# Optimization experiments

Measured on AMD Instinct MI355X. Metric: run time of the kernel, lower is better.

The kernel has to match this reference:

```python
import jax, jax.numpy as jnp
import numpy as np

T = 8  # num_temp_tokens (init arg)
K = 3  # routing conv kernel size (hardcoded in module)


def setup_inputs() -> dict:
    key = jax.random.key(0)
    ks = jax.random.split(key, 7)
    C, CO, NE = 384, 1152, 4
    BT, N = 256, 197
    s = 0.02
    return {
        "x": jax.random.normal(ks[0], (BT, N, C), dtype=jnp.float32),
        "rf_w": jax.random.normal(ks[1], (NE, C), dtype=jnp.float32) * s,
        "rf_b": jax.random.normal(ks[2], (NE,), dtype=jnp.float32) * s,
        "moe_w": jax.random.normal(ks[3], (NE, CO, C, K), dtype=jnp.float32) * s,
        "moe_b": jax.random.normal(ks[4], (NE, CO), dtype=jnp.float32) * s,
        "weight": jax.random.normal(ks[5], (CO, C), dtype=jnp.float32) * s,
        "bias": jax.random.normal(ks[6], (CO,), dtype=jnp.float32) * s,
    }


def _routing(cls, rf_w, rf_b, moe_w, moe_b):
    # cls: (b, C, T). route_func_linear_cls_token_moe forward.
    pooled = cls.mean(axis=2)                       # global avg pool over T -> (b, C)
    rf = pooled @ rf_w.T + rf_b                     # 1x1 conv -> (b, num_experts)
    w = jnp.einsum('be,eock->bock', rf, moe_w)      # per-sample mixed weights (b, 3C, C, K)
    br = rf @ moe_b                                 # per-sample mixed bias (b, 3C)
    clsp = jnp.pad(cls, ((0, 0), (0, 0), (K // 2, K // 2)))
    # sliding windows over T: (b, C, T, K)
    clsw = jnp.stack([clsp[:, :, k:k + cls.shape[2]] for k in range(K)], axis=-1)
    routing = jnp.einsum('bock,bctk->bot', w, clsw) + br[:, :, None] + 1.0  # (b, 3C, T)
    return routing


def reference(x, rf_w, rf_b, moe_w, moe_b, weight, bias):
    bt, n, C = x.shape
    b = bt // T
    xb = x.reshape(b, T, n, C)                      # '(b t) n c -> b t n c'
    cls = xb[:, :, 0, :].transpose(0, 2, 1)         # (b, C, T) cls token stream
    routing = _routing(cls, rf_w, rf_b, moe_w, moe_b)  # (b, 3C, T)
    r = routing.transpose(0, 2, 1)                  # (b, T, 3C)
    rq, rk, rv = jnp.split(r, 3, axis=-1)           # each (b, T, C)
    Wq, Wk, Wv = jnp.split(weight, 3, axis=0)       # each (C, C)
    bq, bk, bv = jnp.split(bias, 3)                 # each (C,)

    def branch(rr, Wc, bc):
        # grouped 1x1 conv with per-(b,t) cin-scaled weight:
        # out[b,t,o,n] = sum_c Wc[o,c] * rr[b,t,c] * x[b,t,n,c] + bc[o]*rr[b,t,o]
        xs = xb * rr[:, :, None, :]                 # (b, T, n, C)
        return jnp.einsum('btnc,oc->bton', xs, Wc) + (bc[None, None, :] * rr)[..., None]

    oq = branch(rq, Wq, bq)
    ok = branch(rk, Wk, bk)
    ov = branch(rv, Wv, bv)
    out = jnp.concatenate([oq, ok, ov], axis=2)     # (b, T, 3C, n)
    return out.reshape(bt, 3 * C, n)
```

## Files before the change

### kernel.cpp

```cpp
#include <hip/hip_runtime.h>
#include <hip/hip_bf16.h>

typedef __attribute__((ext_vector_type(8))) short short8;
typedef __attribute__((ext_vector_type(4))) short short4v;
typedef __attribute__((ext_vector_type(4))) float f32x4;

__device__ __forceinline__ short f2bf(float f) {
    union { float f; unsigned u; } v; v.f = f;
    unsigned r = v.u + 0x7FFF + ((v.u >> 16) & 1);
    return (short)(r >> 16);
}

__device__ __forceinline__ void gll16(const short* g, short* l) {
    __builtin_amdgcn_global_load_lds(
        (const __attribute__((address_space(1))) void*)g,
        (__attribute__((address_space(3))) void*)l, 16, 0, 0);
}

#define NE 4
#define CC 384
#define CO 1152
#define TT 8
#define NN 197
#define NB 32
#define BT 256
#define MOEW_ELEMS 5308416
#define W_ELEMS    442368

__global__ __launch_bounds__(256) void prep_kernel(
    const float* __restrict__ x, const float* __restrict__ rf_w,
    const float* __restrict__ rf_b, const float* __restrict__ moe_w,
    const float* __restrict__ weight,
    short* __restrict__ moeWb, short* __restrict__ Wb,
    short* __restrict__ Yb, float* __restrict__ rf)
{
    int blk = blockIdx.x, tid = threadIdx.x;
    if (blk < NB) {
        __shared__ float clsL[TT * CC];
        __shared__ float pooled[CC];
        int b = blk;
        for (int flat = tid; flat < TT * CC; flat += 256) {
            int t = flat / CC, c = flat - t * CC;
            clsL[flat] = x[(size_t)(b * TT + t) * NN * CC + c];
        }
        __syncthreads();
        for (int c = tid; c < CC; c += 256) {
            float s = 0.f;
            #pragma unroll
            for (int t = 0; t < TT; t++) s += clsL[t * CC + c];
            pooled[c] = s * 0.125f;
        }
        for (int t = 0; t < TT; t++)
            for (int flat = tid; flat < CC * 3; flat += 256) {
                int c = flat / 3, k = flat - c * 3;
                int u = t + k - 1;
                float v = (u >= 0 && u < TT) ? clsL[u * CC + c] : 0.f;
                Yb[(size_t)(b * TT + t) * (CC * 3) + flat] = f2bf(v);
            }
        __syncthreads();
        int wave = tid >> 6, lane = tid & 63;
        float p = 0.f;
        for (int c = lane; c < CC; c += 64) p += pooled[c] * rf_w[wave * CC + c];
        #pragma unroll
        for (int off = 32; off; off >>= 1) p += __shfl_down(p, off, 64);
        if (lane == 0) rf[b * NE + wave] = p + rf_b[wave];
    } else {
        const long NU = (MOEW_ELEMS + W_ELEMS) / 4;
        long step = (long)(gridDim.x - NB) * 256;
        for (long unit = (long)(blk - NB) * 256 + tid; unit < NU; unit += step) {
            long idx = unit * 4;
            float4 v; short* dst;
            if (idx < MOEW_ELEMS) { v = *(const float4*)(moe_w + idx); dst = moeWb + idx; }
            else { long j = idx - MOEW_ELEMS; v = *(const float4*)(weight + j); dst = Wb + j; }
            short4v s;
            s.x = f2bf(v.x); s.y = f2bf(v.y); s.z = f2bf(v.z); s.w = f2bf(v.w);
            *(short4v*)dst = s;
        }
    }
}

__global__ __launch_bounds__(256) void gemm_P(
    const short* __restrict__ A, const short* __restrict__ B, float* __restrict__ P)
{
    __shared__ short A_lds[64 * 64];
    __shared__ short B_lds[64 * 64];
    int bm = blockIdx.x, bn = blockIdx.y, tid = threadIdx.x;
    int wave = tid >> 6, lane = tid & 63, l15 = lane & 15, lq = lane >> 4;
    f32x4 acc[4];
    #pragma unroll
    for (int j = 0; j < 4; j++) acc[j] = (f32x4){0.f, 0.f, 0.f, 0.f};

    for (int kk = 0; kk < 1152 / 64; kk++) {
        __syncthreads();
        #pragma unroll
        for (int j2 = 0; j2 < 2; j2++) {
            int flat = j2 * 256 + tid;
            int row = flat >> 3, seg = flat & 7;
            gll16(A + (size_t)(bm * 64 + row) * 1152 + kk * 64 + seg * 8, &A_lds[flat * 8]);
            gll16(B + (size_t)(bn * 64 + row) * 1152 + kk * 64 + seg * 8, &B_lds[flat * 8]);
        }
        __syncthreads();
        #pragma unroll
        for (int ks = 0; ks < 2; ks++) {
            short8 a = *(short8*)&A_lds[(wave * 16 + l15) * 64 + ks * 32 + lq * 8];
            #pragma unroll
            for (int j = 0; j < 4; j++) {
                short8 bfr = *(short8*)&B_lds[(j * 16 + l15) * 64 + ks * 32 + lq * 8];
                acc[j] = __builtin_amdgcn_mfma_f32_16x16x32_bf16(a, bfr, acc[j], 0, 0, 0);
            }
        }
    }
    #pragma unroll
    for (int j = 0; j < 4; j++)
        #pragma unroll
        for (int reg = 0; reg < 4; reg++) {
            int row = bm * 64 + wave * 16 + lq * 4 + reg;
            int col = bn * 64 + j * 16 + l15;
            P[(size_t)row * 256 + col] = acc[j][reg];
        }
}

__global__ __launch_bounds__(256) void combine_kernel(
    const float* __restrict__ P, const float* __restrict__ rf,
    const float* __restrict__ moe_b, float* __restrict__ r_ws)
{
    __shared__ float rf_l[NB * NE];
    int o = blockIdx.x, tid = threadIdx.x;
    if (tid < NB * NE) rf_l[tid] = rf[tid];
    __syncthreads();
    int b = tid >> 3;
    float acc = 1.0f;
    #pragma unroll
    for (int e = 0; e < NE; e++)
        acc += rf_l[b * NE + e] * (P[(size_t)(e * CO + o) * 256 + tid] + moe_b[e * CO + o]);
    r_ws[(size_t)tid * CO + o] = acc;
}

__global__ __launch_bounds__(256) void main_gemm_fused(
    const float* __restrict__ x, const short* __restrict__ Wb,
    const float* __restrict__ r_ws, const float* __restrict__ bias,
    float* __restrict__ out)
{
    __shared__ short A_lds[2][128 * 32];
    __shared__ short B_lds[2][112 * 32];

    int g = blockIdx.x;
    int u = g & 7, w2 = g >> 3;
    int mt = w2 % 9;
    int pq = u + 8 * (w2 / 9);
    int bt = pq >> 1, nt = pq & 1;
    int tid = threadIdx.x;
    int br = mt / 3;

    const short* Abase = Wb + (size_t)(mt * 128) * CC;

    int wave = tid >> 6, lane = tid & 63, l15 = lane & 15, lq = lane >> 4;
    int oct = tid & 3;
    int rbase = tid >> 2;

    const float* xbase = x + ((size_t)bt * NN + nt * 112) * CC + oct * 8;
    const float* rbp   = r_ws + (size_t)bt * CO + br * CC + oct * 8;

    f32x4 acc[2][7];
    #pragma unroll
    for (int i = 0; i < 2; i++)
        #pragma unroll
        for (int j = 0; j < 7; j++) acc[i][j] = (f32x4){0.f, 0.f, 0.f, 0.f};

    float4 xr[4];
    float4 rr0, rr1;

    auto prefetch = [&](int t) {
        rr0 = *(const float4*)(rbp + t * 32);
        rr1 = *(const float4*)(rbp + t * 32 + 4);
        #pragma unroll
        for (int j2 = 0; j2 < 2; j2++) {
            int row = j2 * 64 + rbase;
            float4 z = {0.f, 0.f, 0.f, 0.f};
            xr[2 * j2] = z; xr[2 * j2 + 1] = z;
            if ((j2 == 0 || rbase < 48) && nt * 112 + row < NN) {
                const float* p = xbase + (size_t)row * CC + t * 32;
                xr[2 * j2]     = *(const float4*)p;
                xr[2 * j2 + 1] = *(const float4*)(p + 4);
            }
        }
    };
    auto issueA = [&](int t, int buf) {
        #pragma unroll
        for (int j2 = 0; j2 < 2; j2++) {
            int flat = j2 * 256 + tid;
            int row = flat >> 2, ss = flat & 3;
            int seg = ss ^ ((row >> 1) & 3);
            gll16(Abase + (size_t)row * CC + t * 32 + seg * 8, &A_lds[buf][flat * 8]);
        }
    };

    prefetch(0);
    issueA(0, 0);

    for (int t = 0; t < 12; t++) {
        int pb = t & 1;
        {
            short* Bd = &B_lds[pb][0];
            #pragma unroll
            for (int j2 = 0; j2 < 2; j2++) {
                int row = j2 * 64 + rbase;
                if (j2 == 0 || rbase < 48) {
                    int ss = oct ^ ((row >> 1) & 3);
                    float4 a = xr[2 * j2], b = xr[2 * j2 + 1];
                    short8 s;
                    s[0] = f2bf(a.x * rr0.x); s[1] = f2bf(a.y * rr0.y);
                    s[2] = f2bf(a.z * rr0.z); s[3] = f2bf(a.w * rr0.w);
                    s[4] = f2bf(b.x * rr1.x); s[5] = f2bf(b.y * rr1.y);
                    s[6] = f2bf(b.z * rr1.z); s[7] = f2bf(b.w * rr1.w);
                    *(short8*)&Bd[row * 32 + ss * 8] = s;
                }
            }
        }
        __syncthreads();
        if (t < 11) {
            prefetch(t + 1);
            issueA(t + 1, pb ^ 1);
        }
        {
            int sx = lq ^ ((l15 >> 1) & 3);
            short8 a0 = *(short8*)&A_lds[pb][(wave * 32      + l15) * 32 + sx * 8];
            short8 a1 = *(short8*)&A_lds[pb][(wave * 32 + 16 + l15) * 32 + sx * 8];
            #pragma unroll
            for (int j = 0; j < 7; j++) {
                short8 bfr = *(short8*)&B_lds[pb][(j * 16 + l15) * 32 + sx * 8];
                acc[0][j] = __builtin_amdgcn_mfma_f32_16x16x32_bf16(a0, bfr, acc[0][j], 0, 0, 0);
                acc[1][j] = __builtin_amdgcn_mfma_f32_16x16x32_bf16(a1, bfr, acc[1][j], 0, 0, 0);
            }
        }
    }

    size_t outbase = (size_t)bt * (CO * NN);
    #pragma unroll
    for (int mi = 0; mi < 2; mi++)
        #pragma unroll
        for (int reg = 0; reg < 4; reg++) {
            int o = mt * 128 + wave * 32 + mi * 16 + lq * 4 + reg;
            float bo = bias[o] * r_ws[(size_t)bt * CO + o];
            #pragma unroll
            for (int j = 0; j < 7; j++) {
                int n = nt * 112 + j * 16 + l15;
                if (n < NN) out[outbase + (size_t)o * NN + n] = acc[mi][j][reg] + bo;
            }
        }
}

extern "C" void kernel_launch(void* const* d_in, const int* in_sizes, int n_in,
                              void* d_out, int out_size, void* d_ws, size_t ws_size,
                              hipStream_t stream) {
    const float* x      = (const float*)d_in[0];
    const float* rf_w   = (const float*)d_in[1];
    const float* rf_b   = (const float*)d_in[2];
    const float* moe_w  = (const float*)d_in[3];
    const float* moe_b  = (const float*)d_in[4];
    const float* weight = (const float*)d_in[5];
    const float* bias   = (const float*)d_in[6];
    float* out = (float*)d_out;

    char* ws = (char*)d_ws;
    short* Wb    = (short*)(ws + 0);
    short* moeWb = (short*)(ws + 884736);
    short* Yb    = (short*)(ws + 11501568);
    float* rf    = (float*)(ws + 12091392);
    float* P     = (float*)(ws + 12091904);
    float* r_ws  = (float*)(ws + 16810496);

    prep_kernel<<<512, 256, 0, stream>>>(x, rf_w, rf_b, moe_w, weight, moeWb, Wb, Yb, rf);
    gemm_P<<<dim3(72, 4), 256, 0, stream>>>(moeWb, Yb, P);
    combine_kernel<<<1152, 256, 0, stream>>>(P, rf, moe_b, r_ws);
    main_gemm_fused<<<4608, 256, 0, stream>>>(x, Wb, r_ws, bias, out);
}
```

Baseline: 451.1 us.

## Split main GEMM tile across 8 waves with 512-thread blocks

The main fused GEMM kernel now launches 512 threads per block instead of 256. Each of the 8 waves computes one 16-row slice of the 128-row output tile instead of two, and the staging and A-load work is spread so each thread handles a single row segment. This halves per-thread accumulators and load work to raise per-block parallelism and latency hiding. The cost is fewer blocks resident per CU, heavier block-wide barriers, and an idle tail of 64 threads during B staging. Each wave also reuses every B fragment for only one MFMA instead of two, so LDS reads per MFMA go up.

Measured after the change: 485.9 us. 7.7% more time.

```diff
diff --git a/kernel.cpp b/kernel.cpp
--- a/kernel.cpp
+++ b/kernel.cpp
@@ -136,7 +136,7 @@
     r_ws[(size_t)tid * CO + o] = acc;
 }
 
-__global__ __launch_bounds__(256) void main_gemm_fused(
+__global__ __launch_bounds__(512) void main_gemm_fused(
     const float* __restrict__ x, const short* __restrict__ Wb,
     const float* __restrict__ r_ws, const float* __restrict__ bias,
     float* __restrict__ out)
@@ -157,41 +157,54 @@
     int wave = tid >> 6, lane = tid & 63, l15 = lane & 15, lq = lane >> 4;
     int oct = tid & 3;
     int rbase = tid >> 2;
+    bool stager = (tid < 448);
 
     const float* xbase = x + ((size_t)bt * NN + nt * 112) * CC + oct * 8;
     const float* rbp   = r_ws + (size_t)bt * CO + br * CC + oct * 8;
 
-    f32x4 acc[2][7];
-    #pragma unroll
-    for (int i = 0; i < 2; i++)
-        #pragma unroll
-        for (int j = 0; j < 7; j++) acc[i][j] = (f32x4){0.f, 0.f, 0.f, 0.f};
-
-    float4 xr[4];
+    f32x4 acc[7];
+    #pragma unroll
+    for (int j = 0; j < 7; j++) acc[j] = (f32x4){0.f, 0.f, 0.f, 0.f};
+
+    float4 xr0, xr1;
     float4 rr0, rr1;
 
     auto prefetch = [&](int t) {
-        rr0 = *(const float4*)(rbp + t * 32);
-        rr1 = *(const float4*)(rbp + t * 32 + 4);
-        #pragma unroll
-        for (int j2 = 0; j2 < 2; j2++) {
-            int row = j2 * 64 + rbase;
+        if (stager) {
+            rr0 = *(const float4*)(rbp + t * 32);
+            rr1 = *(const float4*)(rbp + t * 32 + 4);
             float4 z = {0.f, 0.f, 0.f, 0.f};
-            xr[2 * j2] = z; xr[2 * j2 + 1] = z;
-            if ((j2 == 0 || rbase < 48) && nt * 112 + row < NN) {
-                const float* p = xbase + (size_t)row * CC + t * 32;
-                xr[2 * j2]     = *(const float4*)p;
-                xr[2 * j2 + 1] = *(const float4*)(p + 4);
+            xr0 = z; xr1 = z;
+            if (nt * 112 + rbase < NN) {
+                const float* p = xbase + (size_t)rbase * CC + t * 32;
+                xr0 = *(const float4*)p;
+                xr1 = *(const float4*)(p + 4);
             }
         }
     };
     auto issueA = [&](int t, int buf) {
-        #pragma unroll
-        for (int j2 = 0; j2 < 2; j2++) {
-            int flat = j2 * 256 + tid;
-            int row = flat >> 2, ss = flat & 3;
-            int seg = ss ^ ((row >> 1) & 3);
-            gll16(Abase + (size_t)row * CC + t * 32 + seg * 8, &A_lds[buf][flat * 8]);
+        int row = tid >> 2, ss = tid & 3;
+        int seg = ss ^ ((row >> 1) & 3);
+        gll16(Abase + (size_t)row * CC + t * 32 + seg * 8, &A_lds[buf][tid * 8]);
+    };
+    auto stageB = [&](int pb) {
+        if (stager) {
+            int ss = oct ^ ((rbase >> 1) & 3);
+            short8 s;
+            s[0] = f2bf(xr0.x * rr0.x); s[1] = f2bf(xr0.y * rr0.y);
+            s[2] = f2bf(xr0.z * rr0.z); s[3] = f2bf(xr0.w * rr0.w);
+            s[4] = f2bf(xr1.x * rr1.x); s[5] = f2bf(xr1.y * rr1.y);
+            s[6] = f2bf(xr1.z * rr1.z); s[7] = f2bf(xr1.w * rr1.w);
+            *(short8*)&B_lds[pb][rbase * 32 + ss * 8] = s;
+        }
+    };
+    auto compute = [&](int pb) {
+        int sx = lq ^ ((l15 >> 1) & 3);
+        short8 a = *(short8*)&A_lds[pb][(wave * 16 + l15) * 32 + sx * 8];
+        #pragma unroll
+        for (int j = 0; j < 7; j++) {
+            short8 bfr = *(short8*)&B_lds[pb][(j * 16 + l15) * 32 + sx * 8];
+            acc[j] = __builtin_amdgcn_mfma_f32_16x16x32_bf16(a, bfr, acc[j], 0, 0, 0);
         }
     };
 
@@ -200,54 +213,26 @@
 
     for (int t = 0; t < 12; t++) {
         int pb = t & 1;
-        {
-            short* Bd = &B_lds[pb][0];
-            #pragma unroll
-            for (int j2 = 0; j2 < 2; j2++) {
-                int row = j2 * 64 + rbase;
-                if (j2 == 0 || rbase < 48) {
-                    int ss = oct ^ ((row >> 1) & 3);
-                    float4 a = xr[2 * j2], b = xr[2 * j2 + 1];
-                    short8 s;
-                    s[0] = f2bf(a.x * rr0.x); s[1] = f2bf(a.y * rr0.y);
-                    s[2] = f2bf(a.z * rr0.z); s[3] = f2bf(a.w * rr0.w);
-                    s[4] = f2bf(b.x * rr1.x); s[5] = f2bf(b.y * rr1.y);
-                    s[6] = f2bf(b.z * rr1.z); s[7] = f2bf(b.w * rr1.w);
-                    *(short8*)&Bd[row * 32 + ss * 8] = s;
-                }
-            }
-        }
+        stageB(pb);
         __syncthreads();
         if (t < 11) {
             prefetch(t + 1);
             issueA(t + 1, pb ^ 1);
         }
-        {
-            int sx = lq ^ ((l15 >> 1) & 3);
-            short8 a0 = *(short8*)&A_lds[pb][(wave * 32      + l15) * 32 + sx * 8];
-            short8 a1 = *(short8*)&A_lds[pb][(wave * 32 + 16 + l15) * 32 + sx * 8];
-            #pragma unroll
-            for (int j = 0; j < 7; j++) {
-                short8 bfr = *(short8*)&B_lds[pb][(j * 16 + l15) * 32 + sx * 8];
-                acc[0][j] = __builtin_amdgcn_mfma_f32_16x16x32_bf16(a0, bfr, acc[0][j], 0, 0, 0);
-                acc[1][j] = __builtin_amdgcn_mfma_f32_16x16x32_bf16(a1, bfr, acc[1][j], 0, 0, 0);
-            }
-        }
+        compute(pb);
     }
 
     size_t outbase = (size_t)bt * (CO * NN);
     #pragma unroll
-    for (int mi = 0; mi < 2; mi++)
-        #pragma unroll
-        for (int reg = 0; reg < 4; reg++) {
-            int o = mt * 128 + wave * 32 + mi * 16 + lq * 4 + reg;
-            float bo = bias[o] * r_ws[(size_t)bt * CO + o];
-            #pragma unroll
-            for (int j = 0; j < 7; j++) {
-                int n = nt * 112 + j * 16 + l15;
-                if (n < NN) out[outbase + (size_t)o * NN + n] = acc[mi][j][reg] + bo;
-            }
-        }
+    for (int reg = 0; reg < 4; reg++) {
+        int o = mt * 128 + wave * 16 + lq * 4 + reg;
+        float bo = bias[o] * r_ws[(size_t)bt * CO + o];
+        #pragma unroll
+        for (int j = 0; j < 7; j++) {
+            int n = nt * 112 + j * 16 + l15;
+            if (n < NN) out[outbase + (size_t)o * NN + n] = acc[j][reg] + bo;
+        }
+    }
 }
 
 extern "C" void kernel_launch(void* const* d_in, const int* in_sizes, int n_in,
@@ -273,5 +258,5 @@
     prep_kernel<<<512, 256, 0, stream>>>(x, rf_w, rf_b, moe_w, weight, moeWb, Wb, Yb, rf);
     gemm_P<<<dim3(72, 4), 256, 0, stream>>>(moeWb, Yb, P);
     combine_kernel<<<1152, 256, 0, stream>>>(P, rf, moe_b, r_ws);
-    main_gemm_fused<<<4608, 256, 0, stream>>>(x, Wb, r_ws, bias, out);
-}
+    main_gemm_fused<<<4608, 512, 0, stream>>>(x, Wb, r_ws, bias, out);
+}
```

## Split-K the routing GEMM three ways and use packed bf16 conversion

Applied to the files above, without the earlier changes.

The routing GEMM over the mixed expert weights is split along K into three slices via a third grid dimension, so it launches 864 blocks instead of 288 and fills more compute units. Each slice writes partials to a larger workspace region, and the combine kernel sums them. Separately, the hand-written float-to-bf16 rounding is replaced with the packed v_cvt_pk_bf16_f32 instruction in the weight conversion and in the main GEMM's B staging. This costs extra partial-sum traffic and a bigger workspace.

After: 449.3 us. Within noise of the previous version (-0.4%).

```diff
diff --git a/kernel.cpp b/kernel.cpp
--- a/kernel.cpp
+++ b/kernel.cpp
@@ -9,6 +9,12 @@
     union { float f; unsigned u; } v; v.f = f;
     unsigned r = v.u + 0x7FFF + ((v.u >> 16) & 1);
     return (short)(r >> 16);
+}
+
+__device__ __forceinline__ unsigned cvtpk(float lo, float hi) {
+    unsigned r;
+    asm("v_cvt_pk_bf16_f32 %0, %1, %2" : "=v"(r) : "v"(lo), "v"(hi));
+    return r;
 }
 
 __device__ __forceinline__ void gll16(const short* g, short* l) {
@@ -24,6 +30,7 @@
 #define NN 197
 #define NB 32
 #define BT 256
+#define KS 3
 #define MOEW_ELEMS 5308416
 #define W_ELEMS    442368
 
@@ -72,9 +79,10 @@
             float4 v; short* dst;
             if (idx < MOEW_ELEMS) { v = *(const float4*)(moe_w + idx); dst = moeWb + idx; }
             else { long j = idx - MOEW_ELEMS; v = *(const float4*)(weight + j); dst = Wb + j; }
-            short4v s;
-            s.x = f2bf(v.x); s.y = f2bf(v.y); s.z = f2bf(v.z); s.w = f2bf(v.w);
-            *(short4v*)dst = s;
+            int2 s;
+            s.x = (int)cvtpk(v.x, v.y);
+            s.y = (int)cvtpk(v.z, v.w);
+            *(int2*)dst = s;
         }
     }
 }
@@ -84,13 +92,13 @@
 {
     __shared__ short A_lds[64 * 64];
     __shared__ short B_lds[64 * 64];
-    int bm = blockIdx.x, bn = blockIdx.y, tid = threadIdx.x;
+    int bm = blockIdx.x, bn = blockIdx.y, z = blockIdx.z, tid = threadIdx.x;
     int wave = tid >> 6, lane = tid & 63, l15 = lane & 15, lq = lane >> 4;
     f32x4 acc[4];
     #pragma unroll
     for (int j = 0; j < 4; j++) acc[j] = (f32x4){0.f, 0.f, 0.f, 0.f};
 
-    for (int kk = 0; kk < 1152 / 64; kk++) {
+    for (int kk = z * 6; kk < z * 6 + 6; kk++) {
         __syncthreads();
         #pragma unroll
         for (int j2 = 0; j2 < 2; j2++) {
@@ -116,7 +124,7 @@
         for (int reg = 0; reg < 4; reg++) {
             int row = bm * 64 + wave * 16 + lq * 4 + reg;
             int col = bn * 64 + j * 16 + l15;
-            P[(size_t)row * 256 + col] = acc[j][reg];
+            P[((size_t)z * 4608 + row) * 256 + col] = acc[j][reg];
         }
 }
 
@@ -131,8 +139,13 @@
     int b = tid >> 3;
     float acc = 1.0f;
     #pragma unroll
-    for (int e = 0; e < NE; e++)
-        acc += rf_l[b * NE + e] * (P[(size_t)(e * CO + o) * 256 + tid] + moe_b[e * CO + o]);
+    for (int e = 0; e < NE; e++) {
+        float s = moe_b[e * CO + o];
+        #pragma unroll
+        for (int z = 0; z < KS; z++)
+            s += P[((size_t)z * 4608 + e * CO + o) * 256 + tid];
+        acc += rf_l[b * NE + e] * s;
+    }
     r_ws[(size_t)tid * CO + o] = acc;
 }
 
@@ -194,45 +207,47 @@
             gll16(Abase + (size_t)row * CC + t * 32 + seg * 8, &A_lds[buf][flat * 8]);
         }
     };
+    auto stageB = [&](int pb) {
+        short* Bd = &B_lds[pb][0];
+        #pragma unroll
+        for (int j2 = 0; j2 < 2; j2++) {
+            int row = j2 * 64 + rbase;
+            if (j2 == 0 || rbase < 48) {
+                int ss = oct ^ ((row >> 1) & 3);
+                float4 a = xr[2 * j2], b = xr[2 * j2 + 1];
+                int4 s;
+                s.x = (int)cvtpk(a.x * rr0.x, a.y * rr0.y);
+                s.y = (int)cvtpk(a.z * rr0.z, a.w * rr0.w);
+                s.z = (int)cvtpk(b.x * rr1.x, b.y * rr1.y);
+                s.w = (int)cvtpk(b.z * rr1.z, b.w * rr1.w);
+                *(int4*)&Bd[row * 32 + ss * 8] = s;
+            }
+        }
+    };
+    auto compute = [&](int pb) {
+        int sx = lq ^ ((l15 >> 1) & 3);
+        short8 a0 = *(short8*)&A_lds[pb][(wave * 32      + l15) * 32 + sx * 8];
+        short8 a1 = *(short8*)&A_lds[pb][(wave * 32 + 16 + l15) * 32 + sx * 8];
+        #pragma unroll
+        for (int j = 0; j < 7; j++) {
+            short8 bfr = *(short8*)&B_lds[pb][(j * 16 + l15) * 32 + sx * 8];
+            acc[0][j] = __builtin_amdgcn_mfma_f32_16x16x32_bf16(a0, bfr, acc[0][j], 0, 0, 0);
+            acc[1][j] = __builtin_amdgcn_mfma_f32_16x16x32_bf16(a1, bfr, acc[1][j], 0, 0, 0);
+        }
+    };
 
     prefetch(0);
     issueA(0, 0);
 
     for (int t = 0; t < 12; t++) {
         int pb = t & 1;
-        {
-            short* Bd = &B_lds[pb][0];
-            #pragma unroll
-            for (int j2 = 0; j2 < 2; j2++) {
-                int row = j2 * 64 + rbase;
-                if (j2 == 0 || rbase < 48) {
-                    int ss = oct ^ ((row >> 1) & 3);
-                    float4 a = xr[2 * j2], b = xr[2 * j2 + 1];
-                    short8 s;
-                    s[0] = f2bf(a.x * rr0.x); s[1] = f2bf(a.y * rr0.y);
-                    s[2] = f2bf(a.z * rr0.z); s[3] = f2bf(a.w * rr0.w);
-                    s[4] = f2bf(b.x * rr1.x); s[5] = f2bf(b.y * rr1.y);
-                    s[6] = f2bf(b.z * rr1.z); s[7] = f2bf(b.w * rr1.w);
-                    *(short8*)&Bd[row * 32 + ss * 8] = s;
-                }
-            }
-        }
+        stageB(pb);
         __syncthreads();
         if (t < 11) {
             prefetch(t + 1);
             issueA(t + 1, pb ^ 1);
         }
-        {
-            int sx = lq ^ ((l15 >> 1) & 3);
-            short8 a0 = *(short8*)&A_lds[pb][(wave * 32      + l15) * 32 + sx * 8];
-            short8 a1 = *(short8*)&A_lds[pb][(wave * 32 + 16 + l15) * 32 + sx * 8];
-            #pragma unroll
-            for (int j = 0; j < 7; j++) {
-                short8 bfr = *(short8*)&B_lds[pb][(j * 16 + l15) * 32 + sx * 8];
-                acc[0][j] = __builtin_amdgcn_mfma_f32_16x16x32_bf16(a0, bfr, acc[0][j], 0, 0, 0);
-                acc[1][j] = __builtin_amdgcn_mfma_f32_16x16x32_bf16(a1, bfr, acc[1][j], 0, 0, 0);
-            }
-        }
+        compute(pb);
     }
 
     size_t outbase = (size_t)bt * (CO * NN);
@@ -268,10 +283,10 @@
     short* Yb    = (short*)(ws + 11501568);
     float* rf    = (float*)(ws + 12091392);
     float* P     = (float*)(ws + 12091904);
-    float* r_ws  = (float*)(ws + 16810496);
+    float* r_ws  = (float*)(ws + 26247680);
 
     prep_kernel<<<512, 256, 0, stream>>>(x, rf_w, rf_b, moe_w, weight, moeWb, Wb, Yb, rf);
-    gemm_P<<<dim3(72, 4), 256, 0, stream>>>(moeWb, Yb, P);
+    gemm_P<<<dim3(72, 4, KS), 256, 0, stream>>>(moeWb, Yb, P);
     combine_kernel<<<1152, 256, 0, stream>>>(P, rf, moe_b, r_ws);
     main_gemm_fused<<<4608, 256, 0, stream>>>(x, Wb, r_ws, bias, out);
 }
```
